# Performance work log

Measured on AMD Instinct MI355X. Metric: run time of the kernel, lower is better.

The kernel has to match this reference:

```python
import jax, jax.numpy as jnp
import numpy as np

N = 4096          # number_of_node
DIN = 3           # dim_input (forced: fc1 expects N*dim_input == N*3 after last stage)
DOUT = 4          # dim_output
DACT = N          # dim_action defaults to number_of_node
B = 128


def setup_inputs() -> dict:
    key = jax.random.key(0)
    ks = jax.random.split(key, 12)
    X = jax.random.normal(ks[0], (B, N * DIN), dtype=jnp.float32)
    adj = jax.random.uniform(ks[1], (N, N), dtype=jnp.float32)
    def lin(kw, kb, fan_in, fan_out):
        bound = 1.0 / np.sqrt(fan_in)
        W = jax.random.uniform(kw, (fan_in, fan_out), minval=-bound, maxval=bound, dtype=jnp.float32)
        b = jax.random.uniform(kb, (fan_out,), minval=-bound, maxval=bound, dtype=jnp.float32)
        return W, b
    W1, b1 = lin(ks[2], ks[3], DIN, 4)
    W2, b2 = lin(ks[4], ks[5], 4, DOUT)
    W3, b3 = lin(ks[6], ks[7], DOUT, 3)
    Wfc, bfc = lin(ks[8], ks[9], N * DIN, 54)
    Wout, bout = lin(ks[10], ks[11], 54, DACT)
    return {"X": X, "adj": adj, "W1": W1, "b1": b1, "W2": W2, "b2": b2,
            "W3": W3, "b3": b3, "Wfc": Wfc, "bfc": bfc, "Wout": Wout, "bout": bout}


def reference(X, adj, W1, b1, W2, b2, W3, b3, Wfc, bfc, Wout, bout):
    # X: [B, N*DIN] -> [B, N, DIN]
    h = X.reshape(X.shape[0], N, DIN)
    # three (adj @ h) aggregations fused with tiny Linear + ReLU
    h = jax.nn.relu(jnp.einsum('nm,bmf->bnf', adj, h) @ W1 + b1)   # [B,N,4]
    h = jax.nn.relu(jnp.einsum('nm,bmf->bnf', adj, h) @ W2 + b2)   # [B,N,DOUT]
    h = jax.nn.relu(jnp.einsum('nm,bmf->bnf', adj, h) @ W3 + b3)   # [B,N,3]
    flat = h.reshape(h.shape[0], -1)                               # [B, N*3]
    hid = jax.nn.relu(flat @ Wfc + bfc)                            # [B, 54]
    q_value = hid @ Wout + bout                                    # [B, DACT]
    return q_value
```

## Files before the change

### kernel.cpp

```cpp
#include <hip/hip_runtime.h>


typedef __bf16 bf16x8 __attribute__((ext_vector_type(8)));
typedef float  f32x4  __attribute__((ext_vector_type(4)));

#define N_NODE 4096
#define BATCH  128

__global__ __launch_bounds__(256) void prep_k(const float* __restrict__ adj,
                                              __bf16* __restrict__ adjB,
                                              const float* __restrict__ X,
                                              const float* __restrict__ W1,
                                              __bf16* __restrict__ G0,
                                              float* __restrict__ hid_acc) {
    const int blk = blockIdx.x, tx = threadIdx.x;
    if (blk < 8192) {
        const int g = blk * 256 + tx;
        const int lane = g & 63, ka = (g >> 6) & 127, rb = g >> 13;
        const int row = rb * 16 + (lane & 15);
        const int kb  = ka * 32 + ((lane >> 4) & 3) * 8;
        const float4* s = (const float4*)(adj + (size_t)row * 4096 + kb);
        float4 u = s[0];
        float4 v = s[1];
        bf16x8 o = { (__bf16)u.x, (__bf16)u.y, (__bf16)u.z, (__bf16)u.w,
                     (__bf16)v.x, (__bf16)v.y, (__bf16)v.z, (__bf16)v.w };
        *(bf16x8*)(adjB + (size_t)g * 8) = o;
    } else if (blk < 9216) {
        const int g = (blk - 8192) * 256 + tx;
        const int lp = g & 63, cbg = (g >> 6) & 31, kc = g >> 11;
        const int c = cbg * 16 + (lp & 15);
        const int b = c >> 2, f = c & 3;
        const float w0 = W1[0 * 4 + f], w1 = W1[1 * 4 + f], w2 = W1[2 * 4 + f];
        const int mb = kc * 32 + ((lp >> 4) & 3) * 8;
        const float* Xb = X + (size_t)b * 12288 + (size_t)mb * 3;
        bf16x8 o;
#pragma unroll
        for (int j = 0; j < 8; ++j) {
            const float v = Xb[j * 3 + 0] * w0 + Xb[j * 3 + 1] * w1 + Xb[j * 3 + 2] * w2;
            o[j] = (__bf16)v;
        }
        *(bf16x8*)(G0 + (size_t)g * 8) = o;
    } else {
        const int i = (blk - 9216) * 256 + tx;
        if (i < BATCH * 54) hid_acc[i] = 0.f;
    }
}

template <int MODE>
__global__ __launch_bounds__(256, 2) void gcn_k(const __bf16* __restrict__ A,
                                                const __bf16* __restrict__ Bp,
                                                const float* __restrict__ Wa,
                                                const float* __restrict__ ba,
                                                const float* __restrict__ Wb,
                                                __bf16* __restrict__ Op,
                                                float* __restrict__ hidOut) {
    __shared__ __align__(16) unsigned char smem[65536];
    const int tx = threadIdx.x;
    const int wk = tx >> 6, lane = tx & 63;
    const int quad = lane >> 4, lr = lane & 15;

    const int l = blockIdx.x;
    const int xcd = l & 7, s = l >> 3;
    const int mi = xcd * 8 + (s & 7), ci = s >> 3;
    const int m0 = mi * 64;

    const __bf16* pA[4];
#pragma unroll
    for (int i = 0; i < 4; ++i)
        pA[i] = A + (size_t)(mi * 4 + i) * 65536 + wk * 512 + lane * 8;
    const __bf16* pB[4];
#pragma unroll
    for (int j = 0; j < 4; ++j)
        pB[j] = Bp + (size_t)(wk * 32 + ci * 4 + j) * 512 + lane * 8;

    f32x4 acc[4][4] = {};

#pragma unroll 4
    for (int kt = 0; kt < 32; ++kt) {
        bf16x8 af[4], bv[4];
#pragma unroll
        for (int i = 0; i < 4; ++i)
            af[i] = *(const bf16x8*)(pA[i] + kt * 2048);
#pragma unroll
        for (int j = 0; j < 4; ++j)
            bv[j] = *(const bf16x8*)(pB[j] + kt * 65536);
#pragma unroll
        for (int i = 0; i < 4; ++i)
#pragma unroll
            for (int j = 0; j < 4; ++j)
                acc[i][j] = __builtin_amdgcn_mfma_f32_16x16x32_bf16(
                    af[i], bv[j], acc[i][j], 0, 0, 0);
    }

    float* part = (float*)smem;
#pragma unroll
    for (int t = 0; t < 16; ++t)
        *(f32x4*)(part + wk * 4096 + t * 256 + lane * 4) = acc[t >> 2][t & 3];
    __syncthreads();
    f32x4 fin[4];
#pragma unroll
    for (int u = 0; u < 4; ++u) {
        const int t = wk * 4 + u;
        f32x4 s0 = *(const f32x4*)(part + 0     + t * 256 + lane * 4);
        f32x4 s1 = *(const f32x4*)(part + 4096  + t * 256 + lane * 4);
        f32x4 s2 = *(const f32x4*)(part + 8192  + t * 256 + lane * 4);
        f32x4 s3 = *(const f32x4*)(part + 12288 + t * 256 + lane * 4);
        fin[u] = (s0 + s1) + (s2 + s3);
    }
    __syncthreads();
    float* Ct = (float*)smem;
#pragma unroll
    for (int u = 0; u < 4; ++u)
#pragma unroll
        for (int r = 0; r < 4; ++r)
            Ct[(wk * 16 + quad * 4 + r) * 66 + u * 16 + lr] = fin[u][r];
    __syncthreads();

    if (MODE == 0) {
#pragma unroll
        for (int it = 0; it < 2; ++it) {
            const int g = it * 256 + tx;
            const int lp = g & 63, cbl = (g >> 6) & 3, kcl = g >> 8;
            const int cl = cbl * 16 + (lp & 15);
            const float bf = ba[cl & 3];
            const int mb = kcl * 32 + ((lp >> 4) & 3) * 8;
            bf16x8 o;
#pragma unroll
            for (int j = 0; j < 8; ++j)
                o[j] = (__bf16)fmaxf(Ct[(mb + j) * 66 + cl] + bf, 0.f);
            *(bf16x8*)(Op + ((size_t)((mi * 2 + kcl) * 32 + (ci * 4 + cbl)) * 64 + lp) * 8) = o;
        }
    } else if (MODE == 1) {
        float W2l[16], W3l[12], bl2[4];
#pragma unroll
        for (int i = 0; i < 16; ++i) W2l[i] = Wa[i];
#pragma unroll
        for (int i = 0; i < 12; ++i) W3l[i] = Wb[i];
#pragma unroll
        for (int i = 0; i < 4; ++i) bl2[i] = ba[i];
#pragma unroll
        for (int it = 0; it < 2; ++it) {
            const int g = it * 256 + tx;
            const int lp = g & 63, cbl = (g >> 6) & 3, kcl = g >> 8;
            const int cl = cbl * 16 + (lp & 15);
            const int bloc = cl >> 2, f3 = cl & 3;
            const int mb = kcl * 32 + ((lp >> 4) & 3) * 8;
            bf16x8 o;
#pragma unroll
            for (int j = 0; j < 8; ++j) {
                const float* row = &Ct[(mb + j) * 66 + bloc * 4];
                float v = 0.f;
                if (f3 < 3) {
#pragma unroll
                    for (int fo = 0; fo < 4; ++fo) {
                        const float tmp = fmaxf(row[0] * W2l[fo] + row[1] * W2l[4 + fo] +
                                                row[2] * W2l[8 + fo] + row[3] * W2l[12 + fo] +
                                                bl2[fo], 0.f);
                        const float w3a = W3l[fo * 3 + 0], w3b = W3l[fo * 3 + 1],
                                    w3c = W3l[fo * 3 + 2];
                        v += tmp * (f3 == 0 ? w3a : (f3 == 1 ? w3b : w3c));
                    }
                }
                o[j] = (__bf16)v;
            }
            *(bf16x8*)(Op + ((size_t)((mi * 2 + kcl) * 32 + (ci * 4 + cbl)) * 64 + lp) * 8) = o;
        }
    } else {
        float* red = (float*)(smem + 17408);
        const float b30 = ba[0], b31 = ba[1], b32 = ba[2];
        float accf[16];
#pragma unroll
        for (int b = 0; b < 16; ++b) accf[b] = 0.f;
        if (lane < 54) {
            for (int nn = 0; nn < 16; ++nn) {
                const int n = wk * 16 + nn;
#pragma unroll
                for (int f = 0; f < 3; ++f) {
                    const float w = Wa[((size_t)(m0 + n) * 3 + f) * 54 + lane];
                    const float bf = (f == 0) ? b30 : (f == 1 ? b31 : b32);
#pragma unroll
                    for (int b = 0; b < 16; ++b) {
                        const float r = fmaxf(Ct[n * 66 + b * 4 + f] + bf, 0.f);
                        accf[b] += r * w;
                    }
                }
            }
        }
#pragma unroll
        for (int b = 0; b < 16; ++b) red[(wk * 16 + b) * 64 + lane] = accf[b];
        __syncthreads();
        if (wk == 0 && lane < 54) {
            for (int b = 0; b < 16; ++b) {
                const float s2 = red[b * 64 + lane] + red[(16 + b) * 64 + lane] +
                                 red[(32 + b) * 64 + lane] + red[(48 + b) * 64 + lane];
                atomicAdd(&hidOut[(ci * 16 + b) * 54 + lane], s2);
            }
        }
    }
}

__global__ __launch_bounds__(256) void fc2_k(const float* __restrict__ hid_acc,
                                             const float* __restrict__ bfc,
                                             const float* __restrict__ Wout,
                                             const float* __restrict__ bout,
                                             float* __restrict__ out) {
    const int tx = threadIdx.x;
    const int a  = blockIdx.x * 256 + tx;
    const int b0 = blockIdx.y * 4;
    __shared__ float hs[4 * 54];
    if (tx < 216) {
        const int j = tx % 54;
        hs[tx] = fmaxf(hid_acc[b0 * 54 + tx] + bfc[j], 0.f);
    }
    __syncthreads();
    float a0 = 0.f, a1 = 0.f, a2 = 0.f, a3 = 0.f;
    for (int j = 0; j < 54; ++j) {
        float w = Wout[(size_t)j * N_NODE + a];
        a0 += hs[0 * 54 + j] * w;
        a1 += hs[1 * 54 + j] * w;
        a2 += hs[2 * 54 + j] * w;
        a3 += hs[3 * 54 + j] * w;
    }
    float bo = bout[a];
    out[(size_t)(b0 + 0) * N_NODE + a] = a0 + bo;
    out[(size_t)(b0 + 1) * N_NODE + a] = a1 + bo;
    out[(size_t)(b0 + 2) * N_NODE + a] = a2 + bo;
    out[(size_t)(b0 + 3) * N_NODE + a] = a3 + bo;
}

extern "C" void kernel_launch(void* const* d_in, const int* in_sizes, int n_in,
                              void* d_out, int out_size, void* d_ws, size_t ws_size,
                              hipStream_t stream) {
    const float* X    = (const float*)d_in[0];
    const float* adj  = (const float*)d_in[1];
    const float* W1   = (const float*)d_in[2];
    const float* b1   = (const float*)d_in[3];
    const float* W2   = (const float*)d_in[4];
    const float* b2   = (const float*)d_in[5];
    const float* W3   = (const float*)d_in[6];
    const float* b3   = (const float*)d_in[7];
    const float* Wfc  = (const float*)d_in[8];
    const float* bfc  = (const float*)d_in[9];
    const float* Wout = (const float*)d_in[10];
    const float* bout = (const float*)d_in[11];
    float* out = (float*)d_out;

    char* w = (char*)d_ws;
    __bf16* adjB = (__bf16*)w;
    __bf16* G0   = (__bf16*)(w + 33554432);
    __bf16* H1   = (__bf16*)(w + 33554432 + 4194304);
    __bf16* H2g  = (__bf16*)(w + 33554432 + 2 * 4194304);
    float*  hid  = (float*)(w + 33554432 + 3 * 4194304);

    prep_k<<<9243, 256, 0, stream>>>(adj, adjB, X, W1, G0, hid);

    gcn_k<0><<<512, 256, 0, stream>>>(adjB, G0, nullptr, b1, nullptr, H1, nullptr);
    gcn_k<1><<<512, 256, 0, stream>>>(adjB, H1, W2, b2, W3, H2g, nullptr);
    gcn_k<2><<<512, 256, 0, stream>>>(adjB, H2g, Wfc, b3, nullptr, nullptr, hid);

    fc2_k<<<dim3(16, 32), 256, 0, stream>>>(hid, bfc, Wout, bout, out);
}
```

Before: 218.4 us.

## Split GCN K-reduction across eight waves per block instead of four

Doubles the gcn_k block size to 512 threads, so eight waves each take half as many K iterations of the split-K reduction. The cross-wave partial-sum reduction is restructured into four row passes through a smaller shared buffer, and the epilogues now run one iteration per thread. The aim is more waves per CU to hide memory latency and a shorter serial K loop. In exchange there are more __syncthreads barriers and a wider reduction, and register pressure under launch_bounds(512,4) may cause spills.

```diff
diff --git a/kernel.cpp b/kernel.cpp
--- a/kernel.cpp
+++ b/kernel.cpp
@@ -47,16 +47,16 @@
 }
 
 template <int MODE>
-__global__ __launch_bounds__(256, 2) void gcn_k(const __bf16* __restrict__ A,
+__global__ __launch_bounds__(512, 4) void gcn_k(const __bf16* __restrict__ A,
                                                 const __bf16* __restrict__ Bp,
                                                 const float* __restrict__ Wa,
                                                 const float* __restrict__ ba,
                                                 const float* __restrict__ Wb,
                                                 __bf16* __restrict__ Op,
                                                 float* __restrict__ hidOut) {
-    __shared__ __align__(16) unsigned char smem[65536];
+    __shared__ __align__(16) unsigned char smem[49664];
     const int tx = threadIdx.x;
-    const int wk = tx >> 6, lane = tx & 63;
+    const int wave = tx >> 6, lane = tx & 63;
     const int quad = lane >> 4, lr = lane & 15;
 
     const int l = blockIdx.x;
@@ -67,23 +67,23 @@
     const __bf16* pA[4];
 #pragma unroll
     for (int i = 0; i < 4; ++i)
-        pA[i] = A + (size_t)(mi * 4 + i) * 65536 + wk * 512 + lane * 8;
+        pA[i] = A + (size_t)(mi * 4 + i) * 65536 + wave * 512 + lane * 8;
     const __bf16* pB[4];
 #pragma unroll
     for (int j = 0; j < 4; ++j)
-        pB[j] = Bp + (size_t)(wk * 32 + ci * 4 + j) * 512 + lane * 8;
+        pB[j] = Bp + (size_t)(wave * 32 + (ci * 4 + j)) * 512 + lane * 8;
 
     f32x4 acc[4][4] = {};
 
 #pragma unroll 4
-    for (int kt = 0; kt < 32; ++kt) {
+    for (int kt = 0; kt < 16; ++kt) {
         bf16x8 af[4], bv[4];
 #pragma unroll
         for (int i = 0; i < 4; ++i)
-            af[i] = *(const bf16x8*)(pA[i] + kt * 2048);
+            af[i] = *(const bf16x8*)(pA[i] + kt * 4096);
 #pragma unroll
         for (int j = 0; j < 4; ++j)
-            bv[j] = *(const bf16x8*)(pB[j] + kt * 65536);
+            bv[j] = *(const bf16x8*)(pB[j] + kt * 131072);
 #pragma unroll
         for (int i = 0; i < 4; ++i)
 #pragma unroll
@@ -93,43 +93,37 @@
     }
 
     float* part = (float*)smem;
-#pragma unroll
-    for (int t = 0; t < 16; ++t)
-        *(f32x4*)(part + wk * 4096 + t * 256 + lane * 4) = acc[t >> 2][t & 3];
+    float* Ct   = (float*)(smem + 32768);
+#pragma unroll
+    for (int r = 0; r < 4; ++r) {
+        __syncthreads();
+#pragma unroll
+        for (int u = 0; u < 4; ++u)
+            *(f32x4*)(part + (wave * 4 + u) * 256 + lane * 4) = acc[r][u];
+        __syncthreads();
+        if (wave < 4) {
+            f32x4 fin = {};
+#pragma unroll
+            for (int sl = 0; sl < 8; ++sl)
+                fin += *(const f32x4*)(part + (sl * 4 + wave) * 256 + lane * 4);
+#pragma unroll
+            for (int rr = 0; rr < 4; ++rr)
+                Ct[(r * 16 + quad * 4 + rr) * 66 + wave * 16 + lr] = fin[rr];
+        }
+    }
     __syncthreads();
-    f32x4 fin[4];
-#pragma unroll
-    for (int u = 0; u < 4; ++u) {
-        const int t = wk * 4 + u;
-        f32x4 s0 = *(const f32x4*)(part + 0     + t * 256 + lane * 4);
-        f32x4 s1 = *(const f32x4*)(part + 4096  + t * 256 + lane * 4);
-        f32x4 s2 = *(const f32x4*)(part + 8192  + t * 256 + lane * 4);
-        f32x4 s3 = *(const f32x4*)(part + 12288 + t * 256 + lane * 4);
-        fin[u] = (s0 + s1) + (s2 + s3);
-    }
-    __syncthreads();
-    float* Ct = (float*)smem;
-#pragma unroll
-    for (int u = 0; u < 4; ++u)
-#pragma unroll
-        for (int r = 0; r < 4; ++r)
-            Ct[(wk * 16 + quad * 4 + r) * 66 + u * 16 + lr] = fin[u][r];
-    __syncthreads();
 
     if (MODE == 0) {
-#pragma unroll
-        for (int it = 0; it < 2; ++it) {
-            const int g = it * 256 + tx;
-            const int lp = g & 63, cbl = (g >> 6) & 3, kcl = g >> 8;
-            const int cl = cbl * 16 + (lp & 15);
-            const float bf = ba[cl & 3];
-            const int mb = kcl * 32 + ((lp >> 4) & 3) * 8;
-            bf16x8 o;
-#pragma unroll
-            for (int j = 0; j < 8; ++j)
-                o[j] = (__bf16)fmaxf(Ct[(mb + j) * 66 + cl] + bf, 0.f);
-            *(bf16x8*)(Op + ((size_t)((mi * 2 + kcl) * 32 + (ci * 4 + cbl)) * 64 + lp) * 8) = o;
-        }
+        const int g2 = tx;
+        const int lp = g2 & 63, cbl = (g2 >> 6) & 3, kcl = g2 >> 8;
+        const int cl = cbl * 16 + (lp & 15);
+        const float bf = ba[cl & 3];
+        const int mb = kcl * 32 + ((lp >> 4) & 3) * 8;
+        bf16x8 o;
+#pragma unroll
+        for (int j = 0; j < 8; ++j)
+            o[j] = (__bf16)fmaxf(Ct[(mb + j) * 66 + cl] + bf, 0.f);
+        *(bf16x8*)(Op + ((size_t)((mi * 2 + kcl) * 32 + (ci * 4 + cbl)) * 64 + lp) * 8) = o;
     } else if (MODE == 1) {
         float W2l[16], W3l[12], bl2[4];
 #pragma unroll
@@ -138,42 +132,39 @@
         for (int i = 0; i < 12; ++i) W3l[i] = Wb[i];
 #pragma unroll
         for (int i = 0; i < 4; ++i) bl2[i] = ba[i];
-#pragma unroll
-        for (int it = 0; it < 2; ++it) {
-            const int g = it * 256 + tx;
-            const int lp = g & 63, cbl = (g >> 6) & 3, kcl = g >> 8;
-            const int cl = cbl * 16 + (lp & 15);
-            const int bloc = cl >> 2, f3 = cl & 3;
-            const int mb = kcl * 32 + ((lp >> 4) & 3) * 8;
-            bf16x8 o;
-#pragma unroll
-            for (int j = 0; j < 8; ++j) {
-                const float* row = &Ct[(mb + j) * 66 + bloc * 4];
-                float v = 0.f;
-                if (f3 < 3) {
-#pragma unroll
-                    for (int fo = 0; fo < 4; ++fo) {
-                        const float tmp = fmaxf(row[0] * W2l[fo] + row[1] * W2l[4 + fo] +
-                                                row[2] * W2l[8 + fo] + row[3] * W2l[12 + fo] +
-                                                bl2[fo], 0.f);
-                        const float w3a = W3l[fo * 3 + 0], w3b = W3l[fo * 3 + 1],
-                                    w3c = W3l[fo * 3 + 2];
-                        v += tmp * (f3 == 0 ? w3a : (f3 == 1 ? w3b : w3c));
-                    }
+        const int g2 = tx;
+        const int lp = g2 & 63, cbl = (g2 >> 6) & 3, kcl = g2 >> 8;
+        const int cl = cbl * 16 + (lp & 15);
+        const int bloc = cl >> 2, f3 = cl & 3;
+        const int mb = kcl * 32 + ((lp >> 4) & 3) * 8;
+        bf16x8 o;
+#pragma unroll
+        for (int j = 0; j < 8; ++j) {
+            const float* row = &Ct[(mb + j) * 66 + bloc * 4];
+            float v = 0.f;
+            if (f3 < 3) {
+#pragma unroll
+                for (int fo = 0; fo < 4; ++fo) {
+                    const float tmp = fmaxf(row[0] * W2l[fo] + row[1] * W2l[4 + fo] +
+                                            row[2] * W2l[8 + fo] + row[3] * W2l[12 + fo] +
+                                            bl2[fo], 0.f);
+                    const float w3a = W3l[fo * 3 + 0], w3b = W3l[fo * 3 + 1],
+                                w3c = W3l[fo * 3 + 2];
+                    v += tmp * (f3 == 0 ? w3a : (f3 == 1 ? w3b : w3c));
                 }
-                o[j] = (__bf16)v;
             }
-            *(bf16x8*)(Op + ((size_t)((mi * 2 + kcl) * 32 + (ci * 4 + cbl)) * 64 + lp) * 8) = o;
-        }
+            o[j] = (__bf16)v;
+        }
+        *(bf16x8*)(Op + ((size_t)((mi * 2 + kcl) * 32 + (ci * 4 + cbl)) * 64 + lp) * 8) = o;
     } else {
-        float* red = (float*)(smem + 17408);
+        float* red = part;
         const float b30 = ba[0], b31 = ba[1], b32 = ba[2];
         float accf[16];
 #pragma unroll
         for (int b = 0; b < 16; ++b) accf[b] = 0.f;
         if (lane < 54) {
-            for (int nn = 0; nn < 16; ++nn) {
-                const int n = wk * 16 + nn;
+            for (int nn = 0; nn < 8; ++nn) {
+                const int n = wave * 8 + nn;
 #pragma unroll
                 for (int f = 0; f < 3; ++f) {
                     const float w = Wa[((size_t)(m0 + n) * 3 + f) * 54 + lane];
@@ -187,12 +178,15 @@
             }
         }
 #pragma unroll
-        for (int b = 0; b < 16; ++b) red[(wk * 16 + b) * 64 + lane] = accf[b];
+        for (int b = 0; b < 16; ++b)
+            red[(wave * 16 + b) * 64 + lane] = accf[b];
         __syncthreads();
-        if (wk == 0 && lane < 54) {
+        if (wave == 0 && lane < 54) {
             for (int b = 0; b < 16; ++b) {
-                const float s2 = red[b * 64 + lane] + red[(16 + b) * 64 + lane] +
-                                 red[(32 + b) * 64 + lane] + red[(48 + b) * 64 + lane];
+                float s2 = 0.f;
+#pragma unroll
+                for (int w8 = 0; w8 < 8; ++w8)
+                    s2 += red[(w8 * 16 + b) * 64 + lane];
                 atomicAdd(&hidOut[(ci * 16 + b) * 54 + lane], s2);
             }
         }
@@ -254,9 +248,9 @@
 
     prep_k<<<9243, 256, 0, stream>>>(adj, adjB, X, W1, G0, hid);
 
-    gcn_k<0><<<512, 256, 0, stream>>>(adjB, G0, nullptr, b1, nullptr, H1, nullptr);
-    gcn_k<1><<<512, 256, 0, stream>>>(adjB, H1, W2, b2, W3, H2g, nullptr);
-    gcn_k<2><<<512, 256, 0, stream>>>(adjB, H2g, Wfc, b3, nullptr, nullptr, hid);
+    gcn_k<0><<<512, 512, 0, stream>>>(adjB, G0, nullptr, b1, nullptr, H1, nullptr);
+    gcn_k<1><<<512, 512, 0, stream>>>(adjB, H1, W2, b2, W3, H2g, nullptr);
+    gcn_k<2><<<512, 512, 0, stream>>>(adjB, H2g, Wfc, b3, nullptr, nullptr, hid);
 
     fc2_k<<<dim3(16, 32), 256, 0, stream>>>(hid, bfc, Wout, bout, out);
 }
```

New measurement: 209.2 us. 4.2% less time.
